# Optimization experiments

Hardware: AMD Instinct MI355X
Metric: run time of the kernel (lower is better)

The kernel has to match this reference:

```python
import jax, jax.numpy as jnp
import numpy as np

B, D, L, T, K = 16, 256, 256, 1000, 3
DW, DC = 4, 2  # dim_w, dim_c
CH = 8         # ConvSwishBlock out channels (10 = 1 start + 1 end + 8)


def swish(x):
    return x * jax.nn.sigmoid(x)


def setup_inputs() -> dict:
    key = jax.random.key(0)
    ks = jax.random.split(key, 12)
    # durations ~ U[1,6] per phone -> sum ~ 3.5*L ~ 896 <= T
    durations = 1.0 + 5.0 * jax.random.uniform(ks[0], (B, L), dtype=jnp.float32)
    phoneme = jax.random.normal(ks[1], (B, D, L), dtype=jnp.float32)
    # True = padded phone position
    phone_len = L - (jnp.arange(B) % 4) * 16
    phoneme_mask = (jnp.arange(L)[None, :] >= phone_len[:, None])[:, None, :]
    durations = jnp.where(phoneme_mask[:, 0, :], 0.0, durations)
    s = 0.02
    p = {
        'proj_w_W': s * jax.random.normal(ks[2], (D, D)), 'proj_w_b': jnp.zeros((D,)),
        'conv_w_W': s * jax.random.normal(ks[3], (CH, D, K)), 'conv_w_b': jnp.zeros((CH,)),
        'mlp_w_W': s * jax.random.normal(ks[4], (2 + CH, DW)), 'mlp_w_b': jnp.zeros((DW,)),
        'lin_w_W': s * jax.random.normal(ks[5], (D * DW, D)), 'lin_w_b': jnp.zeros((D,)),
        'proj_c_W': s * jax.random.normal(ks[6], (D, D)), 'proj_c_b': jnp.zeros((D,)),
        'conv_c_W': s * jax.random.normal(ks[7], (CH, D, K)), 'conv_c_b': jnp.zeros((CH,)),
        'mlp_c_W': s * jax.random.normal(ks[8], (2 + CH, DC)), 'mlp_c_b': jnp.zeros((DC,)),
        'lin_c_W': s * jax.random.normal(ks[9], (DW * DC, D)), 'lin_c_b': jnp.zeros((D,)),
    }
    return {'durations': durations, 'phoneme': phoneme, 'phoneme_mask': phoneme_mask, **p}


def _conv_branch(x, phone_pad, projW, projb, convW, convb):
    # x: (B, D, L). 1x1 conv projection, then K-wide 'same' conv to CH channels, swish, mask.
    x = jnp.einsum('od,bdl->bol', projW, x) + projb[None, :, None]
    h = jax.lax.conv_general_dilated(x, convW, (1,), 'SAME',
                                     dimension_numbers=('NCH', 'OIH', 'NCH'))
    h = swish(h + convb[None, :, None])
    h = jnp.where(phone_pad[:, None, :], 0.0, h)
    return h.transpose(0, 2, 1)  # (B, L, CH)


def _forward(durations, phoneme, phoneme_mask,
             proj_w_W, proj_w_b, conv_w_W, conv_w_b, mlp_w_W, mlp_w_b, lin_w_W, lin_w_b,
             proj_c_W, proj_c_b, conv_c_W, conv_c_b, mlp_c_W, mlp_c_b, lin_c_W, lin_c_b):
    phone_pad = phoneme_mask[:, 0, :]                       # (B, L) True = pad
    frame_len = jnp.clip(jnp.round(jnp.sum(durations, -1)), 0, T).astype(jnp.int32)
    frame_pad = jnp.arange(T)[None, :] >= frame_len[:, None]  # (B, T) True = pad
    attn_pad = frame_pad[:, :, None] | phone_pad[:, None, :]  # (B, T, L)

    sd = jnp.cumsum(durations, -1)                          # (B, L) cumulative end times
    sk = sd - durations                                     # (B, L) start times
    t = jnp.arange(1, T + 1, dtype=durations.dtype)
    S = jnp.where(attn_pad, 0.0, t[None, :, None] - sk[:, None, :])                    # (B,T,L)
    E = jnp.where(attn_pad, 0.0, jnp.broadcast_to(sd[:, None, :], attn_pad.shape)
                  - sk[:, None, :])                                                    # (B,T,L)

    # W branch: per-(frame, phone) attention weights over phones
    h_w = _conv_branch(phoneme, phone_pad, proj_w_W, proj_w_b, conv_w_W, conv_w_b)     # (B,L,CH)
    feat_w = jnp.concatenate(
        [S[..., None], E[..., None], jnp.broadcast_to(h_w[:, None], (B, T, L, CH))], -1)
    w = swish(feat_w @ mlp_w_W + mlp_w_b)                   # (B, T, L, DW)
    w = jnp.where(phone_pad[:, None, :, None], -jnp.inf, w)
    w = jax.nn.softmax(w, axis=2)                           # softmax over phones
    w = jnp.where(frame_pad[:, :, None, None], 0.0, w)

    # C branch: auxiliary per-(frame, phone) context
    h_c = _conv_branch(phoneme, phone_pad, proj_c_W, proj_c_b, conv_c_W, conv_c_b)
    feat_c = jnp.concatenate(
        [S[..., None], E[..., None], jnp.broadcast_to(h_c[:, None], (B, T, L, CH))], -1)
    c = swish(feat_c @ mlp_c_W + mlp_c_b)                   # (B, T, L, DC)

    # combine: wh = einsum over phones with phoneme features, wc with c matrix
    wh = jnp.einsum('btnq,bnh->btqh', w, phoneme.transpose(0, 2, 1))  # (B,T,DW,D)
    wh = wh.reshape(B, T, DW * D) @ lin_w_W + lin_w_b                 # (B,T,D)
    wc = jnp.einsum('btnq,btnp->btqp', w, c)                          # (B,T,DW,DC)
    wc = wc.reshape(B, T, DW * DC) @ lin_c_W + lin_c_b                # (B,T,D)
    return wh + wc


def reference(durations, phoneme, phoneme_mask,
              proj_w_W, proj_w_b, conv_w_W, conv_w_b, mlp_w_W, mlp_w_b, lin_w_W, lin_w_b,
              proj_c_W, proj_c_b, conv_c_W, conv_c_b, mlp_c_W, mlp_c_b, lin_c_W, lin_c_b):
    return _forward(durations, phoneme, phoneme_mask,
                    proj_w_W, proj_w_b, conv_w_W, conv_w_b, mlp_w_W, mlp_w_b, lin_w_W, lin_w_b,
                    proj_c_W, proj_c_b, conv_c_W, conv_c_b, mlp_c_W, mlp_c_b, lin_c_W, lin_c_b)
```

## Files before the change

kernel.cpp:

```cpp
#include <hip/hip_runtime.h>


typedef short v8s __attribute__((ext_vector_type(8)));
typedef _Float16 v8h __attribute__((ext_vector_type(8)));
typedef float f4 __attribute__((ext_vector_type(4)));

__device__ __forceinline__ float bf2f(unsigned short h) {
  return __uint_as_float(((unsigned int)h) << 16);
}
__device__ __forceinline__ unsigned short f2bf(float f) {
  unsigned int u = __float_as_uint(f);
  u = (u + 0x7FFFu + ((u >> 16) & 1u)) >> 16;
  return (unsigned short)u;
}
__device__ __forceinline__ float swishf(float x) {
  return x * __builtin_amdgcn_rcpf(1.f + __expf(-x));
}

__global__ __launch_bounds__(256) void k_prep(
    const float* __restrict__ dur, const float* __restrict__ ph,
    const float* __restrict__ liWw,
    const float* __restrict__ cvWw, const float* __restrict__ pjWw,
    const float* __restrict__ pjbw,
    const float* __restrict__ cvWc, const float* __restrict__ pjWc,
    const float* __restrict__ pjbc,
    float* __restrict__ sk, int* __restrict__ frame_len,
    unsigned short* __restrict__ Mb, float* __restrict__ bK,
    unsigned short* __restrict__ LWT, unsigned short* __restrict__ phT) {
  __shared__ float sm[32 * 33];
  int blk = blockIdx.x, tid = threadIdx.x;
  if (blk < 16) {
    int b = blk, l = tid;
    float d = dur[b * 256 + l];
    sm[l] = d;
    __syncthreads();
    for (int off = 1; off < 256; off <<= 1) {
      float v = (l >= off) ? sm[l - off] : 0.f;
      __syncthreads();
      sm[l] += v;
      __syncthreads();
    }
    sk[b * 256 + l] = sm[l] - d;
    if (l == 255) {
      int fl = (int)rintf(sm[255]);
      frame_len[b] = min(max(fl, 0), 1000);
    }
  } else if (blk < 64) {
    int x = blk - 16;
    int br = x / 24, ck = x % 24;
    int ch = ck / 3, k = ck % 3;
    const float* convW = br ? cvWc : cvWw;
    const float* projW = br ? pjWc : pjWw;
    const float* projb = br ? pjbc : pjbw;
    int d = tid;
    float a0 = 0.f, a1 = 0.f, a2 = 0.f, a3 = 0.f;
    for (int o = 0; o < 256; o += 4) {
      a0 += convW[ch * 768 + (o + 0) * 3 + k] * projW[(o + 0) * 256 + d];
      a1 += convW[ch * 768 + (o + 1) * 3 + k] * projW[(o + 1) * 256 + d];
      a2 += convW[ch * 768 + (o + 2) * 3 + k] * projW[(o + 2) * 256 + d];
      a3 += convW[ch * 768 + (o + 3) * 3 + k] * projW[(o + 3) * 256 + d];
    }
    Mb[(br * 24 + ck) * 256 + d] = f2bf((a0 + a1) + (a2 + a3));
    if (tid < 64) {
      float pb = 0.f;
      for (int o = tid; o < 256; o += 64)
        pb += convW[ch * 768 + o * 3 + k] * projb[o];
#pragma unroll
      for (int off = 1; off < 64; off <<= 1) pb += __shfl_xor(pb, off);
      if (tid == 0) bK[br * 24 + ck] = pb;
    }
  } else if (blk < 320) {
    int idx = blk - 64;
    int kt = idx & 31, ot = idx >> 5;
    int tx = tid & 31, ty = tid >> 5;
#pragma unroll
    for (int r = 0; r < 4; r++) {
      int row = ty + r * 8;
      sm[row * 33 + tx] = liWw[(size_t)(kt * 32 + row) * 256 + ot * 32 + tx];
    }
    __syncthreads();
#pragma unroll
    for (int r = 0; r < 4; r++) {
      int row = ty + r * 8;
      LWT[(size_t)(ot * 32 + row) * 1024 + kt * 32 + tx] =
          f2bf(sm[tx * 33 + row]);
    }
  } else {
    int idx = blk - 320;
    int ht = idx & 7, lt = (idx >> 3) & 7, b = idx >> 6;
    int tx = tid & 31, ty = tid >> 5;
#pragma unroll
    for (int r = 0; r < 4; r++) {
      int row = ty + r * 8;
      sm[row * 33 + tx] =
          ph[(size_t)b * 65536 + (size_t)(ht * 32 + row) * 256 + lt * 32 + tx];
    }
    __syncthreads();
#pragma unroll
    for (int r = 0; r < 4; r++) {
      int row = ty + r * 8;
      phT[(size_t)b * 65536 + (size_t)(lt * 32 + row) * 256 + ht * 32 + tx] =
          f2bf(sm[tx * 33 + row]);
    }
  }
}

__global__ __launch_bounds__(256) void k_convG(
    const unsigned short* __restrict__ phT, const unsigned short* __restrict__ Mb,
    const float* __restrict__ bK, const float* __restrict__ cvbw,
    const float* __restrict__ cvbc, const float* __restrict__ dur,
    const float* __restrict__ sk, const float* __restrict__ mlpWw,
    const float* __restrict__ mlpbw, const float* __restrict__ mlpWc,
    const float* __restrict__ mlpbc, const unsigned short* __restrict__ LWT,
    float* __restrict__ Lbw, float* __restrict__ Laux,
    float* __restrict__ maxAb, _Float16* __restrict__ G) {
  __shared__ __align__(16) float C[256 * 49];
  __shared__ float redm[4][4];
  int blk = blockIdx.x;
  int tid = threadIdx.x, wave = tid >> 6, lane = tid & 63;
  int quad = lane >> 4, col = lane & 15;
  if (blk < 16) {
    int b = blk;
    int l0 = wave * 64;
    const unsigned short* Ab = phT + (size_t)b * 65536;
    f4 acc[4][3] = {};
#pragma unroll
    for (int k0 = 0; k0 < 256; k0 += 32) {
      v8s af[4], bf[3];
#pragma unroll
      for (int lt = 0; lt < 4; lt++)
        af[lt] = *(const v8s*)(Ab + (size_t)(l0 + lt * 16 + col) * 256 + k0 + quad * 8);
#pragma unroll
      for (int ct = 0; ct < 3; ct++)
        bf[ct] = *(const v8s*)(Mb + (size_t)(ct * 16 + col) * 256 + k0 + quad * 8);
#pragma unroll
      for (int lt = 0; lt < 4; lt++)
#pragma unroll
        for (int ct = 0; ct < 3; ct++)
          acc[lt][ct] = __builtin_amdgcn_mfma_f32_16x16x32_bf16(af[lt], bf[ct],
                                                                acc[lt][ct], 0, 0, 0);
    }
#pragma unroll
    for (int lt = 0; lt < 4; lt++)
#pragma unroll
      for (int ct = 0; ct < 3; ct++)
#pragma unroll
        for (int r = 0; r < 4; r++)
          C[(l0 + lt * 16 + quad * 4 + r) * 49 + ct * 16 + col] = acc[lt][ct][r];
    __syncthreads();
    int l = tid;
    float dv = dur[b * 256 + l];
    bool vld = (dv != 0.f);
    float hv[2][8];
#pragma unroll
    for (int br = 0; br < 2; br++) {
      const float* convb = br ? cvbc : cvbw;
#pragma unroll
      for (int ch = 0; ch < 8; ch++) {
        int ck = br * 24 + ch * 3;
        float v = convb[ch] + bK[ck + 1] + C[l * 49 + ck + 1];
        if (l > 0) v += bK[ck + 0] + C[(l - 1) * 49 + ck + 0];
        if (l < 255) v += bK[ck + 2] + C[(l + 1) * 49 + ck + 2];
        hv[br][ch] = vld ? swishf(v) : 0.f;
      }
    }
    float skl = sk[b * 256 + l];
    float A[4];
#pragma unroll
    for (int q = 0; q < 4; q++) {
      float a = mlpbw[q] + dv * mlpWw[4 + q] - skl * mlpWw[q];
#pragma unroll
      for (int ch = 0; ch < 8; ch++) a += hv[0][ch] * mlpWw[(2 + ch) * 4 + q];
      A[q] = vld ? a : -1e30f;
    }
    float bb0 = mlpbc[0] + dv * mlpWc[2] - skl * mlpWc[0];
    float bb1 = mlpbc[1] + dv * mlpWc[3] - skl * mlpWc[1];
#pragma unroll
    for (int ch = 0; ch < 8; ch++) {
      bb0 += hv[1][ch] * mlpWc[(2 + ch) * 2 + 0];
      bb1 += hv[1][ch] * mlpWc[(2 + ch) * 2 + 1];
    }
    float4 Av = {A[0], A[1], A[2], A[3]};
    ((float4*)Lbw)[b * 256 + l] = Av;
    float4 Xv = {bb0, bb1, vld ? 1.f : 0.f, 0.f};
    ((float4*)Laux)[b * 256 + l] = Xv;
    float m0 = A[0], m1 = A[1], m2 = A[2], m3 = A[3];
#pragma unroll
    for (int off = 1; off < 64; off <<= 1) {
      m0 = fmaxf(m0, __shfl_xor(m0, off));
      m1 = fmaxf(m1, __shfl_xor(m1, off));
      m2 = fmaxf(m2, __shfl_xor(m2, off));
      m3 = fmaxf(m3, __shfl_xor(m3, off));
    }
    if (lane == 0) {
      redm[wave][0] = m0;
      redm[wave][1] = m1;
      redm[wave][2] = m2;
      redm[wave][3] = m3;
    }
    __syncthreads();
    if (tid < 4)
      maxAb[b * 4 + tid] = fmaxf(fmaxf(redm[0][tid], redm[1][tid]),
                                 fmaxf(redm[2][tid], redm[3][tid]));
  } else {
    int idx = blk - 16;
    int b = (idx & 7) * 2 + ((idx >> 3) & 1);
    int sub = idx >> 4;
    int q = sub >> 3, rem = sub & 7;
    int mo = (rem >> 2) * 128, nl = (rem & 3) * 64;
    int wm = (wave & 1) * 64, wn = (wave >> 1) * 32;
    const unsigned short* Ag = LWT + (size_t)q * 256;
    const unsigned short* Bg = phT + (size_t)b * 65536;
    size_t aoff[4], boff[2];
#pragma unroll
    for (int mt = 0; mt < 4; mt++)
      aoff[mt] = (size_t)(mo + wm + mt * 16 + col) * 1024 + quad * 8;
#pragma unroll
    for (int nt = 0; nt < 2; nt++)
      boff[nt] = (size_t)(nl + wn + nt * 16 + col) * 256 + quad * 8;

    v8s ra[2][4], rb[2][2];
#pragma unroll
    for (int c = 0; c < 2; c++) {
#pragma unroll
      for (int mt = 0; mt < 4; mt++)
        ra[c][mt] = *(const v8s*)(Ag + aoff[mt] + c * 32);
#pragma unroll
      for (int nt = 0; nt < 2; nt++)
        rb[c][nt] = *(const v8s*)(Bg + boff[nt] + c * 32);
    }
    f4 acc[4][2] = {};
#pragma unroll
    for (int s = 0; s < 8; s++) {
#pragma unroll
      for (int mt = 0; mt < 4; mt++)
#pragma unroll
        for (int nt = 0; nt < 2; nt++)
          acc[mt][nt] = __builtin_amdgcn_mfma_f32_16x16x32_bf16(
              ra[s & 1][mt], rb[s & 1][nt], acc[mt][nt], 0, 0, 0);
      if (s < 6) {
#pragma unroll
        for (int mt = 0; mt < 4; mt++)
          ra[s & 1][mt] = *(const v8s*)(Ag + aoff[mt] + (s + 2) * 32);
#pragma unroll
        for (int nt = 0; nt < 2; nt++)
          rb[s & 1][nt] = *(const v8s*)(Bg + boff[nt] + (s + 2) * 32);
      }
    }
    _Float16* Gb = G + (size_t)b * 262144 + q * 256;
#pragma unroll
    for (int mt = 0; mt < 4; mt++)
#pragma unroll
      for (int r = 0; r < 4; r++) {
        int orow = mo + wm + mt * 16 + quad * 4 + r;
#pragma unroll
        for (int nt = 0; nt < 2; nt++) {
          int lcol = nl + wn + nt * 16 + col;
          Gb[(size_t)orow * 1024 + lcol] = (_Float16)acc[mt][nt][r];
        }
      }
  }
}

__global__ __launch_bounds__(512, 4) void k_fuse(
    const float* __restrict__ Lbw, const float* __restrict__ Laux,
    const float* __restrict__ maxAb, const int* __restrict__ frame_len,
    const float* __restrict__ mlpWw, const float* __restrict__ mlpWc,
    const _Float16* __restrict__ G, const float* __restrict__ lwb,
    const float* __restrict__ lcb, const float* __restrict__ LC,
    float* __restrict__ out) {
  __shared__ __align__(16) _Float16 Asm[32 * 512];
  __shared__ __align__(16) float4 Lb4[272];
  __shared__ __align__(16) float4 Lx4[272];
  __shared__ float bias_s[256];
  __shared__ float lcs[8][256];
  __shared__ float wcs[32][8];

  int idx = blockIdx.x;
  int b = (idx & 7) * 2 + ((idx >> 3) & 1);
  int t0 = (idx >> 4) * 32;
  int tid = threadIdx.x, wave = tid >> 6, lane = tid & 63;
  int quad = lane >> 4, col = lane & 15;

  int fl = frame_len[b];
  if (t0 >= fl) {
    int o = tid & 255;
    float v = lwb[o] + lcb[o];
    for (int r = tid >> 8; r < 32; r += 2) {
      int t = t0 + r;
      if (t < 1000) out[((size_t)(b * 1000 + t)) * 256 + o] = v;
    }
    return;
  }

  if (tid < 256) {
    float4 av = ((const float4*)Lbw)[b * 256 + tid];
    float4 xv = ((const float4*)Laux)[b * 256 + tid];
    int li = tid + (tid >> 4);
    Lb4[li] = av;
    Lx4[li] = xv;
    bias_s[tid] = lwb[tid] + lcb[tid];
  }
  for (int i = tid; i < 2048; i += 512) lcs[i >> 8][i & 255] = LC[i];

  float4 mx4 = ((const float4*)maxAb)[b];
  float mw0 = mlpWw[0], mw1 = mlpWw[1], mw2 = mlpWw[2], mw3 = mlpWw[3];
  float mc0 = mlpWc[0], mc1 = mlpWc[1];

  int l_grp = lane & 15;
  int row = wave * 4 + (lane >> 4);
  int t = t0 + row;
  bool live = (t < fl);
  float tp1 = (float)(t + 1);
  int rsw = row & 7;
  int asw = col & 7;
  int wn = wave * 32;
  f4 acc[2][2] = {};

  const _Float16* GA =
      G + (size_t)b * 262144 + (size_t)(wn + col) * 1024 + quad * 8;
  const _Float16* GB = GA + (size_t)16 * 1024;

  __syncthreads();

  float cpa[16], cpb[16];
#pragma unroll
  for (int j = 0; j < 16; ++j) {
    int l = l_grp * 16 + j;
    int li = l + (l >> 4);
    float4 ax = Lx4[li];
    cpa[j] = swishf(ax.x + tp1 * mc0);
    cpb[j] = swishf(ax.y + tp1 * mc1);
  }

#pragma unroll
  for (int p = 0; p < 2; ++p) {
    const _Float16* GpA = GA + p * 512;
    const _Float16* GpB = GB + p * 512;
    v8h rb[4][2];
#pragma unroll
    for (int c = 0; c < 4; ++c) {
      rb[c][0] = *(const v8h*)(GpA + c * 32);
      rb[c][1] = *(const v8h*)(GpB + c * 32);
    }

    float mq0 = p ? mw2 : mw0;
    float mq1 = p ? mw3 : mw1;
    float mxa = p ? mx4.z : mx4.x;
    float mxb = p ? mx4.w : mx4.y;
    float m0 = live ? fmaxf(mxa + tp1 * mq0, 0.f) : 1e30f;
    float m1 = live ? fmaxf(mxb + tp1 * mq1, 0.f) : 1e30f;
    float s0 = 0.f, s1 = 0.f, p00 = 0.f, p01 = 0.f, p10 = 0.f, p11 = 0.f;
    v8h e0[2], e1[2];
#pragma unroll
    for (int j = 0; j < 16; ++j) {
      int l = l_grp * 16 + j;
      int li = l + (l >> 4);
      float4 A4 = Lb4[li];
      float zz = ((const float*)&Lx4[li])[2];
      float Aq0 = p ? A4.z : A4.x;
      float Aq1 = p ? A4.w : A4.y;
      _Float16 eh0 = (_Float16)(__expf(swishf(Aq0 + tp1 * mq0) - m0) * zz);
      _Float16 eh1 = (_Float16)(__expf(swishf(Aq1 + tp1 * mq1) - m1) * zz);
      e0[j >> 3][j & 7] = eh0;
      e1[j >> 3][j & 7] = eh1;
      float f0 = (float)eh0, f1 = (float)eh1;
      s0 += f0;
      s1 += f1;
      p00 += f0 * cpa[j];
      p01 += f0 * cpb[j];
      p10 += f1 * cpa[j];
      p11 += f1 * cpb[j];
    }
#pragma unroll
    for (int off = 1; off < 16; off <<= 1) {
      s0 += __shfl_xor(s0, off);
      s1 += __shfl_xor(s1, off);
      p00 += __shfl_xor(p00, off);
      p01 += __shfl_xor(p01, off);
      p10 += __shfl_xor(p10, off);
      p11 += __shfl_xor(p11, off);
    }
    float iv0 = live ? 1.0f / s0 : 0.f;
    float iv1 = live ? 1.0f / s1 : 0.f;

    if (p) __syncthreads();

    if (l_grp == 0) {
      wcs[row][p * 4 + 0] = p00 * iv0;
      wcs[row][p * 4 + 1] = p01 * iv0;
      wcs[row][p * 4 + 2] = p10 * iv1;
      wcs[row][p * 4 + 3] = p11 * iv1;
    }
#pragma unroll
    for (int c = 0; c < 2; ++c) {
      int sl = (l_grp * 2 + c) ^ rsw;
      v8h w0, w1;
#pragma unroll
      for (int k = 0; k < 8; ++k) {
        w0[k] = (_Float16)((float)e0[c][k] * iv0);
        w1[k] = (_Float16)((float)e1[c][k] * iv1);
      }
      *(v8h*)&Asm[(row * 64 + sl) * 8] = w0;
      *(v8h*)&Asm[(row * 64 + 32 + sl) * 8] = w1;
    }
    __syncthreads();
    __builtin_amdgcn_s_setprio(1);
#pragma unroll
    for (int s = 0; s < 16; ++s) {
      int slk = s * 4 + quad;
      v8h af0 = *(const v8h*)&Asm[(col * 64 + (slk ^ asw)) * 8];
      v8h af1 = *(const v8h*)&Asm[((16 + col) * 64 + (slk ^ asw)) * 8];
      acc[0][0] = __builtin_amdgcn_mfma_f32_16x16x32_f16(af0, rb[s & 3][0],
                                                         acc[0][0], 0, 0, 0);
      acc[1][0] = __builtin_amdgcn_mfma_f32_16x16x32_f16(af1, rb[s & 3][0],
                                                         acc[1][0], 0, 0, 0);
      acc[0][1] = __builtin_amdgcn_mfma_f32_16x16x32_f16(af0, rb[s & 3][1],
                                                         acc[0][1], 0, 0, 0);
      acc[1][1] = __builtin_amdgcn_mfma_f32_16x16x32_f16(af1, rb[s & 3][1],
                                                         acc[1][1], 0, 0, 0);
      if (s < 12) {
        rb[s & 3][0] = *(const v8h*)(GpA + (s + 4) * 32);
        rb[s & 3][1] = *(const v8h*)(GpB + (s + 4) * 32);
      }
    }
    __builtin_amdgcn_s_setprio(0);
  }
#pragma unroll
  for (int mt = 0; mt < 2; ++mt)
#pragma unroll
    for (int r = 0; r < 4; ++r) {
      int lrow = mt * 16 + quad * 4 + r;
      int trow = t0 + lrow;
      if (trow < 1000) {
        float4 wa = *(const float4*)&wcs[lrow][0];
        float4 wb = *(const float4*)&wcs[lrow][4];
        float wcl[8] = {wa.x, wa.y, wa.z, wa.w, wb.x, wb.y, wb.z, wb.w};
#pragma unroll
        for (int nt = 0; nt < 2; ++nt) {
          int oc = wn + nt * 16 + col;
          float v = acc[mt][nt][r] + bias_s[oc];
#pragma unroll
          for (int jj = 0; jj < 8; ++jj) v = fmaf(wcl[jj], lcs[jj][oc], v);
          out[((size_t)(b * 1000 + trow)) * 256 + oc] = v;
        }
      }
    }
}

extern "C" void kernel_launch(void* const* d_in, const int* in_sizes, int n_in,
                              void* d_out, int out_size, void* d_ws, size_t ws_size,
                              hipStream_t stream) {
  const float* dur  = (const float*)d_in[0];
  const float* ph   = (const float*)d_in[1];
  const float* pjWw = (const float*)d_in[3];
  const float* pjbw = (const float*)d_in[4];
  const float* cvWw = (const float*)d_in[5];
  const float* cvbw = (const float*)d_in[6];
  const float* mlWw = (const float*)d_in[7];
  const float* mlbw = (const float*)d_in[8];
  const float* liWw = (const float*)d_in[9];
  const float* libw = (const float*)d_in[10];
  const float* pjWc = (const float*)d_in[11];
  const float* pjbc = (const float*)d_in[12];
  const float* cvWc = (const float*)d_in[13];
  const float* cvbc = (const float*)d_in[14];
  const float* mlWc = (const float*)d_in[15];
  const float* mlbc = (const float*)d_in[16];
  const float* liWc = (const float*)d_in[17];
  const float* libc = (const float*)d_in[18];
  float* out = (float*)d_out;

  float* f = (float*)d_ws;
  size_t o = 0;
  float* sk = f + o;            o += 4096;
  int* fl = (int*)(f + o);      o += 16;
  float* bK = f + o;            o += 64;
  unsigned short* Mb = (unsigned short*)(f + o); o += 6144;
  float* Lbw = f + o;           o += 16384;
  float* Laux = f + o;          o += 16384;
  float* mxA = f + o;           o += 64;
  _Float16* G = (_Float16*)(f + o);              o += 2097152;
  unsigned short* phT = (unsigned short*)(f + o); o += 524288;
  unsigned short* LWT = (unsigned short*)(f + o); o += 131072;

  k_prep<<<1344, 256, 0, stream>>>(dur, ph, liWw, cvWw, pjWw, pjbw, cvWc, pjWc,
                                   pjbc, sk, fl, Mb, bK, LWT, phT);
  k_convG<<<528, 256, 0, stream>>>(phT, Mb, bK, cvbw, cvbc, dur, sk, mlWw,
                                   mlbw, mlWc, mlbc, LWT, Lbw, Laux, mxA, G);
  k_fuse<<<512, 512, 0, stream>>>(Lbw, Laux, mxA, fl, mlWw, mlWc, G, libw,
                                  libc, liWc, out);
}
```

Baseline: 180.3 us.

## Double k_fuse time tile to 64 rows with 1024-thread blocks

Each k_fuse block now covers 64 time frames with 16 waves, and each wave owns 16 output columns across four M tiles instead of 32 columns across two. This halves how often each block's G (phoneme-projection) fragments are reloaded per time frame, and halves the grid to 256 blocks. The per-thread precomputed cpa/cpb arrays are dropped and recomputed inside the softmax loop to save registers. In exchange the block uses more LDS and has fewer, larger blocks, which may worsen load balance since blocks past frame_len exit early.

```diff
diff --git a/kernel.cpp b/kernel.cpp
--- a/kernel.cpp
+++ b/kernel.cpp
@@ -262,23 +262,23 @@
   }
 }
 
-__global__ __launch_bounds__(512, 4) void k_fuse(
+__global__ __launch_bounds__(1024, 4) void k_fuse(
     const float* __restrict__ Lbw, const float* __restrict__ Laux,
     const float* __restrict__ maxAb, const int* __restrict__ frame_len,
     const float* __restrict__ mlpWw, const float* __restrict__ mlpWc,
     const _Float16* __restrict__ G, const float* __restrict__ lwb,
     const float* __restrict__ lcb, const float* __restrict__ LC,
     float* __restrict__ out) {
-  __shared__ __align__(16) _Float16 Asm[32 * 512];
+  __shared__ __align__(16) _Float16 Asm[64 * 512];
   __shared__ __align__(16) float4 Lb4[272];
   __shared__ __align__(16) float4 Lx4[272];
   __shared__ float bias_s[256];
   __shared__ float lcs[8][256];
-  __shared__ float wcs[32][8];
+  __shared__ float wcs[64][8];
 
   int idx = blockIdx.x;
   int b = (idx & 7) * 2 + ((idx >> 3) & 1);
-  int t0 = (idx >> 4) * 32;
+  int t0 = (idx >> 4) * 64;
   int tid = threadIdx.x, wave = tid >> 6, lane = tid & 63;
   int quad = lane >> 4, col = lane & 15;
 
@@ -286,7 +286,7 @@
   if (t0 >= fl) {
     int o = tid & 255;
     float v = lwb[o] + lcb[o];
-    for (int r = tid >> 8; r < 32; r += 2) {
+    for (int r = tid >> 8; r < 64; r += 4) {
       int t = t0 + r;
       if (t < 1000) out[((size_t)(b * 1000 + t)) * 256 + o] = v;
     }
@@ -301,7 +301,7 @@
     Lx4[li] = xv;
     bias_s[tid] = lwb[tid] + lcb[tid];
   }
-  for (int i = tid; i < 2048; i += 512) lcs[i >> 8][i & 255] = LC[i];
+  for (int i = tid; i < 2048; i += 1024) lcs[i >> 8][i & 255] = LC[i];
 
   float4 mx4 = ((const float4*)maxAb)[b];
   float mw0 = mlpWw[0], mw1 = mlpWw[1], mw2 = mlpWw[2], mw3 = mlpWw[3];
@@ -314,35 +314,20 @@
   float tp1 = (float)(t + 1);
   int rsw = row & 7;
   int asw = col & 7;
-  int wn = wave * 32;
-  f4 acc[2][2] = {};
+  int wn = wave * 16;
+  f4 acc[4] = {};
 
   const _Float16* GA =
       G + (size_t)b * 262144 + (size_t)(wn + col) * 1024 + quad * 8;
-  const _Float16* GB = GA + (size_t)16 * 1024;
 
   __syncthreads();
 
-  float cpa[16], cpb[16];
-#pragma unroll
-  for (int j = 0; j < 16; ++j) {
-    int l = l_grp * 16 + j;
-    int li = l + (l >> 4);
-    float4 ax = Lx4[li];
-    cpa[j] = swishf(ax.x + tp1 * mc0);
-    cpb[j] = swishf(ax.y + tp1 * mc1);
-  }
-
 #pragma unroll
   for (int p = 0; p < 2; ++p) {
-    const _Float16* GpA = GA + p * 512;
-    const _Float16* GpB = GB + p * 512;
-    v8h rb[4][2];
-#pragma unroll
-    for (int c = 0; c < 4; ++c) {
-      rb[c][0] = *(const v8h*)(GpA + c * 32);
-      rb[c][1] = *(const v8h*)(GpB + c * 32);
-    }
+    const _Float16* Gp = GA + p * 512;
+    v8h rb[4];
+#pragma unroll
+    for (int c = 0; c < 4; ++c) rb[c] = *(const v8h*)(Gp + c * 32);
 
     float mq0 = p ? mw2 : mw0;
     float mq1 = p ? mw3 : mw1;
@@ -357,20 +342,22 @@
       int l = l_grp * 16 + j;
       int li = l + (l >> 4);
       float4 A4 = Lb4[li];
-      float zz = ((const float*)&Lx4[li])[2];
+      float4 ax = Lx4[li];
+      float cp0 = swishf(ax.x + tp1 * mc0);
+      float cp1 = swishf(ax.y + tp1 * mc1);
       float Aq0 = p ? A4.z : A4.x;
       float Aq1 = p ? A4.w : A4.y;
-      _Float16 eh0 = (_Float16)(__expf(swishf(Aq0 + tp1 * mq0) - m0) * zz);
-      _Float16 eh1 = (_Float16)(__expf(swishf(Aq1 + tp1 * mq1) - m1) * zz);
+      _Float16 eh0 = (_Float16)(__expf(swishf(Aq0 + tp1 * mq0) - m0) * ax.z);
+      _Float16 eh1 = (_Float16)(__expf(swishf(Aq1 + tp1 * mq1) - m1) * ax.z);
       e0[j >> 3][j & 7] = eh0;
       e1[j >> 3][j & 7] = eh1;
       float f0 = (float)eh0, f1 = (float)eh1;
       s0 += f0;
       s1 += f1;
-      p00 += f0 * cpa[j];
-      p01 += f0 * cpb[j];
-      p10 += f1 * cpa[j];
-      p11 += f1 * cpb[j];
+      p00 += f0 * cp0;
+      p01 += f0 * cp1;
+      p10 += f1 * cp0;
+      p11 += f1 * cp1;
     }
 #pragma unroll
     for (int off = 1; off < 16; off <<= 1) {
@@ -409,25 +396,20 @@
 #pragma unroll
     for (int s = 0; s < 16; ++s) {
       int slk = s * 4 + quad;
-      v8h af0 = *(const v8h*)&Asm[(col * 64 + (slk ^ asw)) * 8];
-      v8h af1 = *(const v8h*)&Asm[((16 + col) * 64 + (slk ^ asw)) * 8];
-      acc[0][0] = __builtin_amdgcn_mfma_f32_16x16x32_f16(af0, rb[s & 3][0],
-                                                         acc[0][0], 0, 0, 0);
-      acc[1][0] = __builtin_amdgcn_mfma_f32_16x16x32_f16(af1, rb[s & 3][0],
-                                                         acc[1][0], 0, 0, 0);
-      acc[0][1] = __builtin_amdgcn_mfma_f32_16x16x32_f16(af0, rb[s & 3][1],
-                                                         acc[0][1], 0, 0, 0);
-      acc[1][1] = __builtin_amdgcn_mfma_f32_16x16x32_f16(af1, rb[s & 3][1],
-                                                         acc[1][1], 0, 0, 0);
-      if (s < 12) {
-        rb[s & 3][0] = *(const v8h*)(GpA + (s + 4) * 32);
-        rb[s & 3][1] = *(const v8h*)(GpB + (s + 4) * 32);
-      }
+      v8h af[4];
+#pragma unroll
+      for (int mt = 0; mt < 4; ++mt)
+        af[mt] = *(const v8h*)&Asm[((mt * 16 + col) * 64 + (slk ^ asw)) * 8];
+#pragma unroll
+      for (int mt = 0; mt < 4; ++mt)
+        acc[mt] = __builtin_amdgcn_mfma_f32_16x16x32_f16(af[mt], rb[s & 3],
+                                                         acc[mt], 0, 0, 0);
+      if (s < 12) rb[s & 3] = *(const v8h*)(Gp + (s + 4) * 32);
     }
     __builtin_amdgcn_s_setprio(0);
   }
 #pragma unroll
-  for (int mt = 0; mt < 2; ++mt)
+  for (int mt = 0; mt < 4; ++mt)
 #pragma unroll
     for (int r = 0; r < 4; ++r) {
       int lrow = mt * 16 + quad * 4 + r;
@@ -436,14 +418,11 @@
         float4 wa = *(const float4*)&wcs[lrow][0];
         float4 wb = *(const float4*)&wcs[lrow][4];
         float wcl[8] = {wa.x, wa.y, wa.z, wa.w, wb.x, wb.y, wb.z, wb.w};
-#pragma unroll
-        for (int nt = 0; nt < 2; ++nt) {
-          int oc = wn + nt * 16 + col;
-          float v = acc[mt][nt][r] + bias_s[oc];
-#pragma unroll
-          for (int jj = 0; jj < 8; ++jj) v = fmaf(wcl[jj], lcs[jj][oc], v);
-          out[((size_t)(b * 1000 + trow)) * 256 + oc] = v;
-        }
+        int oc = wn + col;
+        float v = acc[mt][r] + bias_s[oc];
+#pragma unroll
+        for (int jj = 0; jj < 8; ++jj) v = fmaf(wcl[jj], lcs[jj][oc], v);
+        out[((size_t)(b * 1000 + trow)) * 256 + oc] = v;
       }
     }
 }
@@ -488,6 +467,6 @@
                                    pjbc, sk, fl, Mb, bK, LWT, phT);
   k_convG<<<528, 256, 0, stream>>>(phT, Mb, bK, cvbw, cvbc, dur, sk, mlWw,
                                    mlbw, mlWc, mlbc, LWT, Lbw, Laux, mxA, G);
-  k_fuse<<<512, 512, 0, stream>>>(Lbw, Laux, mxA, fl, mlWw, mlWc, G, libw,
-                                  libc, liWc, out);
-}
+  k_fuse<<<256, 1024, 0, stream>>>(Lbw, Laux, mxA, fl, mlWw, mlWc, G, libw,
+                                   libc, liWc, out);
+}
```

New measurement: 173.2 us. 4.0% less time.
